# Kernel tuning notes

Measured on AMD Instinct MI355X. Metric: run time of the kernel, lower is better.

Reference implementation:

```python
import jax, jax.numpy as jnp
import numpy as np

N = 50000
E = 800000
IN = 256
HEADS = 8
C = 32  # out_size // heads
OUT = HEADS * C
NEG_SLOPE = 0.2
LN_EPS = 1e-5


def setup_inputs() -> dict:
    key = jax.random.key(0)
    ks = jax.random.split(key, 6)
    x = jax.random.normal(ks[0], (N, IN), dtype=jnp.float32)
    edge_index = jax.random.randint(ks[1], (2, E), 0, N, dtype=jnp.int64)
    W = jax.random.normal(ks[2], (IN, OUT), dtype=jnp.float32) / np.sqrt(IN)
    att_src = jax.random.normal(ks[3], (HEADS, C), dtype=jnp.float32) / np.sqrt(C)
    att_dst = jax.random.normal(ks[4], (HEADS, C), dtype=jnp.float32) / np.sqrt(C)
    bias = jnp.zeros((OUT,), dtype=jnp.float32)
    ln_gamma = jnp.ones((OUT,), dtype=jnp.float32)
    ln_beta = jnp.zeros((OUT,), dtype=jnp.float32)
    return {"x": x, "edge_index": edge_index, "W": W, "att_src": att_src,
            "att_dst": att_dst, "bias": bias, "ln_gamma": ln_gamma, "ln_beta": ln_beta}


def _gat_layer(x, src, dst, W, att_src, att_dst, bias, ln_gamma, ln_beta):
    n = x.shape[0]
    h = (x @ W).reshape(n, HEADS, C)                      # [N,H,C]
    a_src = jnp.sum(h * att_src[None], axis=-1)           # [N,H]
    a_dst = jnp.sum(h * att_dst[None], axis=-1)           # [N,H]
    e = a_src[src] + a_dst[dst]                           # [Etot,H]
    e = jnp.where(e > 0, e, NEG_SLOPE * e)                # LeakyReLU(0.2)
    # segment softmax over incoming edges of each dst node
    emax = jax.lax.stop_gradient(jax.ops.segment_max(e, dst, num_segments=n))
    ex = jnp.exp(e - emax[dst])
    denom = jax.ops.segment_sum(ex, dst, num_segments=n)
    alpha = ex / denom[dst]                               # [Etot,H]
    msg = h[src] * alpha[:, :, None]                      # [Etot,H,C]
    out = jax.ops.segment_sum(msg, dst, num_segments=n).reshape(n, OUT) + bias
    # LayerNorm
    mu = jnp.mean(out, axis=-1, keepdims=True)
    var = jnp.var(out, axis=-1, keepdims=True)
    out = (out - mu) * jax.lax.rsqrt(var + LN_EPS) * ln_gamma + ln_beta
    return jax.nn.relu(out)


def reference(x, edge_index, W, att_src, att_dst, bias, ln_gamma, ln_beta):
    n = x.shape[0]
    loops = jnp.arange(n, dtype=edge_index.dtype)
    src = jnp.concatenate([edge_index[0], loops])  # PyG GATConv adds self-loops
    dst = jnp.concatenate([edge_index[1], loops])
    return _gat_layer(x, src, dst, W, att_src, att_dst, bias, ln_gamma, ln_beta)
```

## Files before the change

### kernel.cpp

```cpp
#include <hip/hip_runtime.h>

#define NEG 0.2f
#define ELLW 64

typedef __attribute__((ext_vector_type(8))) __bf16 bf16x8;
typedef __attribute__((ext_vector_type(4))) float f32x4;

__device__ __forceinline__ unsigned short f2bf(float f) {
    unsigned int u = __float_as_uint(f);
    u += 0x7FFFu + ((u >> 16) & 1u);
    return (unsigned short)(u >> 16);
}

__global__ __launch_bounds__(256) void prep_kernel(const float* __restrict__ W,
                                                   unsigned short* __restrict__ Wt,
                                                   int* __restrict__ len, int N) {
    int n = blockIdx.x, k = threadIdx.x;
    Wt[n * 256 + k] = f2bf(W[k * 256 + n]);
    int idx = n * 256 + k;
    if (idx < N) len[idx] = 0;
}

struct SmemGemm { unsigned short A[64][40]; unsigned short B[256][40]; };
struct SmemEpi  { float asrc[64][9]; float adst[64][9]; };
union SmemU { SmemGemm g; SmemEpi e; };

__global__ __launch_bounds__(256) void gemm_ell(const float* __restrict__ x,
                                                const unsigned short* __restrict__ Wt,
                                                unsigned short* __restrict__ h,
                                                const float* __restrict__ att_src,
                                                const float* __restrict__ att_dst,
                                                float* __restrict__ a_src,
                                                float* __restrict__ a_dst, int nrows, int G,
                                                const int* __restrict__ ei,
                                                int* __restrict__ len,
                                                int* __restrict__ ell, int E) {
    __shared__ SmemU sm;

    if (blockIdx.x >= G) {
        int e = (blockIdx.x - G) * 256 + threadIdx.x;
        if (e < E) {
            int s = ei[e], d = ei[E + e];
            int slot = atomicAdd(&len[d], 1);
            if (slot < ELLW) ell[d * ELLW + slot] = s;
        }
        return;
    }

    int t = threadIdx.x;
    int lane = t & 63, wave = t >> 6;
    int row0 = blockIdx.x * 64;

    f32x4 acc[4][4] = {};

    for (int kk = 0; kk < 8; ++kk) {
        int k0 = kk * 32;
        {
            int r = t >> 2, cg = (t & 3) * 8;
            int gr = row0 + r;
            float4 v0 = make_float4(0.f, 0.f, 0.f, 0.f), v1 = v0;
            if (gr < nrows) {
                const float* p = x + (size_t)gr * 256 + k0 + cg;
                v0 = *(const float4*)p;
                v1 = *(const float4*)(p + 4);
            }
            unsigned long long p0 = (unsigned long long)f2bf(v0.x)
                                  | ((unsigned long long)f2bf(v0.y) << 16)
                                  | ((unsigned long long)f2bf(v0.z) << 32)
                                  | ((unsigned long long)f2bf(v0.w) << 48);
            unsigned long long p1 = (unsigned long long)f2bf(v1.x)
                                  | ((unsigned long long)f2bf(v1.y) << 16)
                                  | ((unsigned long long)f2bf(v1.z) << 32)
                                  | ((unsigned long long)f2bf(v1.w) << 48);
            *(unsigned long long*)&sm.g.A[r][cg]     = p0;
            *(unsigned long long*)&sm.g.A[r][cg + 4] = p1;
        }
        {
            const uint4* src = (const uint4*)(Wt + (size_t)t * 256 + k0);
            uint4 b0 = src[0], b1 = src[1], b2 = src[2], b3 = src[3];
            *(uint4*)&sm.g.B[t][0]  = b0;
            *(uint4*)&sm.g.B[t][8]  = b1;
            *(uint4*)&sm.g.B[t][16] = b2;
            *(uint4*)&sm.g.B[t][24] = b3;
        }
        __syncthreads();

        int fr = lane & 15, fk = (lane >> 4) * 8;
        bf16x8 a[4];
#pragma unroll
        for (int mi = 0; mi < 4; ++mi) a[mi] = *(const bf16x8*)&sm.g.A[mi * 16 + fr][fk];
#pragma unroll
        for (int ni = 0; ni < 4; ++ni) {
            bf16x8 b = *(const bf16x8*)&sm.g.B[wave * 64 + ni * 16 + fr][fk];
#pragma unroll
            for (int mi = 0; mi < 4; ++mi)
                acc[mi][ni] = __builtin_amdgcn_mfma_f32_16x16x32_bf16(a[mi], b, acc[mi][ni], 0, 0, 0);
        }
        __syncthreads();
    }

    int cr = (lane >> 4) * 4;
    int cc = lane & 15;
#pragma unroll
    for (int mi = 0; mi < 4; ++mi)
#pragma unroll
        for (int ni = 0; ni < 4; ++ni)
#pragma unroll
            for (int r = 0; r < 4; ++r) {
                int row = row0 + mi * 16 + cr + r;
                int col = wave * 64 + ni * 16 + cc;
                if (row < nrows) h[(size_t)row * 256 + col] = f2bf(acc[mi][ni][r]);
            }

    float avs[4], avd[4];
#pragma unroll
    for (int ni = 0; ni < 4; ++ni) {
        int col = wave * 64 + ni * 16 + cc;
        avs[ni] = att_src[col];
        avd[ni] = att_dst[col];
    }
#pragma unroll
    for (int mi = 0; mi < 4; ++mi)
#pragma unroll
        for (int r = 0; r < 4; ++r) {
            float s0 = acc[mi][0][r] * avs[0] + acc[mi][1][r] * avs[1];
            float s1 = acc[mi][2][r] * avs[2] + acc[mi][3][r] * avs[3];
            float d0 = acc[mi][0][r] * avd[0] + acc[mi][1][r] * avd[1];
            float d1 = acc[mi][2][r] * avd[2] + acc[mi][3][r] * avd[3];
#pragma unroll
            for (int o = 1; o < 16; o <<= 1) {
                s0 += __shfl_xor(s0, o, 64);
                s1 += __shfl_xor(s1, o, 64);
                d0 += __shfl_xor(d0, o, 64);
                d1 += __shfl_xor(d1, o, 64);
            }
            if (cc == 0) {
                int row = mi * 16 + cr + r;
                sm.e.asrc[row][wave * 2 + 0] = s0;
                sm.e.asrc[row][wave * 2 + 1] = s1;
                sm.e.adst[row][wave * 2 + 0] = d0;
                sm.e.adst[row][wave * 2 + 1] = d1;
            }
        }
    __syncthreads();
    for (int idx = t; idx < 512; idx += 256) {
        int row = idx >> 3, hd = idx & 7;
        if (row0 + row < nrows) {
            a_src[(size_t)(row0 + row) * 8 + hd] = sm.e.asrc[row][hd];
            a_dst[(size_t)(row0 + row) * 8 + hd] = sm.e.adst[row][hd];
        }
    }
}

__global__ __launch_bounds__(256) void agg_kernel(const unsigned short* __restrict__ h,
                                                  const float* __restrict__ a_src,
                                                  const float* __restrict__ a_dst,
                                                  const int* __restrict__ len,
                                                  const int* __restrict__ ell,
                                                  const float* __restrict__ bias,
                                                  const float* __restrict__ gamma,
                                                  const float* __restrict__ beta,
                                                  float* __restrict__ out) {
    int i = blockIdx.x;
    int t = threadIdx.x;
    int lane = t & 63, wave = t >> 6;
    int hh = t & 7, jj = t >> 3;
    int deg = len[i];
    deg = deg < ELLW ? deg : ELLW;

    __shared__ float al_buf[ELLW][8];
    __shared__ int   s_buf[ELLW];
    __shared__ float wred[4][8];
    __shared__ float ginv[8];
    __shared__ float al_self[8];
    __shared__ float partial[8][256];
    __shared__ float lnred[4][2];

    float adh = a_dst[i * 8 + hh];
    float es = a_src[i * 8 + hh] + adh;
    es = es > 0.f ? es : NEG * es;
    float esx = __expf(es);
    float sm = (jj == 0) ? esx : 0.f;
    if (t < 8) al_self[t] = esx;

#pragma unroll
    for (int it = 0; it < 2; ++it) {
        int j = it * 32 + jj;
        if (j < deg) {
            int s = ell[i * ELLW + j];
            if (hh == 0) s_buf[j] = s;
            float e = a_src[s * 8 + hh] + adh;
            e = e > 0.f ? e : NEG * e;
            float v = __expf(e);
            al_buf[j][hh] = v;
            sm += v;
        }
    }
    sm += __shfl_xor(sm, 8, 64);
    sm += __shfl_xor(sm, 16, 64);
    sm += __shfl_xor(sm, 32, 64);
    if (lane < 8) wred[wave][lane] = sm;
    __syncthreads();
    if (t < 8) ginv[t] = 1.0f / (wred[0][t] + wred[1][t] + wred[2][t] + wred[3][t]);
    __syncthreads();

    int sub = lane >> 5, l5 = lane & 31;
    int p = wave * 2 + sub;
    int c0 = l5 * 8;
    int hl = l5 >> 2;
    float invd = ginv[hl];
    f32x4 a0 = {0.f, 0.f, 0.f, 0.f}, a1 = {0.f, 0.f, 0.f, 0.f};
    for (int j = p; j < deg; j += 8) {
        int s = s_buf[j];
        float alpha = al_buf[j][hl] * invd;
        uint4 u = *(const uint4*)(h + (size_t)s * 256 + c0);
        a0[0] = fmaf(alpha, __uint_as_float(u.x << 16), a0[0]);
        a0[1] = fmaf(alpha, __uint_as_float(u.x & 0xffff0000u), a0[1]);
        a0[2] = fmaf(alpha, __uint_as_float(u.y << 16), a0[2]);
        a0[3] = fmaf(alpha, __uint_as_float(u.y & 0xffff0000u), a0[3]);
        a1[0] = fmaf(alpha, __uint_as_float(u.z << 16), a1[0]);
        a1[1] = fmaf(alpha, __uint_as_float(u.z & 0xffff0000u), a1[1]);
        a1[2] = fmaf(alpha, __uint_as_float(u.w << 16), a1[2]);
        a1[3] = fmaf(alpha, __uint_as_float(u.w & 0xffff0000u), a1[3]);
    }
    if (p == 7) {
        float alpha = al_self[hl] * invd;
        uint4 u = *(const uint4*)(h + (size_t)i * 256 + c0);
        a0[0] = fmaf(alpha, __uint_as_float(u.x << 16), a0[0]);
        a0[1] = fmaf(alpha, __uint_as_float(u.x & 0xffff0000u), a0[1]);
        a0[2] = fmaf(alpha, __uint_as_float(u.y << 16), a0[2]);
        a0[3] = fmaf(alpha, __uint_as_float(u.y & 0xffff0000u), a0[3]);
        a1[0] = fmaf(alpha, __uint_as_float(u.z << 16), a1[0]);
        a1[1] = fmaf(alpha, __uint_as_float(u.z & 0xffff0000u), a1[1]);
        a1[2] = fmaf(alpha, __uint_as_float(u.w << 16), a1[2]);
        a1[3] = fmaf(alpha, __uint_as_float(u.w & 0xffff0000u), a1[3]);
    }
    *(f32x4*)&partial[p][c0]     = a0;
    *(f32x4*)&partial[p][c0 + 4] = a1;
    __syncthreads();

    float o = bias[t];
#pragma unroll
    for (int q = 0; q < 8; ++q) o += partial[q][t];

    float s1 = o, s2 = o * o;
#pragma unroll
    for (int off = 32; off >= 1; off >>= 1) {
        s1 += __shfl_xor(s1, off, 64);
        s2 += __shfl_xor(s2, off, 64);
    }
    if (lane == 0) { lnred[wave][0] = s1; lnred[wave][1] = s2; }
    __syncthreads();
    float S1 = lnred[0][0] + lnred[1][0] + lnred[2][0] + lnred[3][0];
    float S2 = lnred[0][1] + lnred[1][1] + lnred[2][1] + lnred[3][1];
    float mean = S1 * (1.f / 256.f);
    float var = S2 * (1.f / 256.f) - mean * mean;
    float rstd = rsqrtf(var + 1e-5f);
    float val = (o - mean) * rstd * gamma[t] + beta[t];
    val = fmaxf(val, 0.f);
    out[(size_t)i * 256 + t] = val;
}

extern "C" void kernel_launch(void* const* d_in, const int* in_sizes, int n_in,
                              void* d_out, int out_size, void* d_ws, size_t ws_size,
                              hipStream_t stream) {
    const float* x       = (const float*)d_in[0];
    const int*   ei      = (const int*)d_in[1];
    const float* W       = (const float*)d_in[2];
    const float* att_src = (const float*)d_in[3];
    const float* att_dst = (const float*)d_in[4];
    const float* bias    = (const float*)d_in[5];
    const float* gamma   = (const float*)d_in[6];
    const float* beta    = (const float*)d_in[7];

    int N = in_sizes[0] / 256;
    int E = in_sizes[1] / 2;
    int G = (N + 63) / 64;
    int EB = (E + 255) / 256;

    char* ws = (char*)d_ws;
    size_t off = 0;
    auto alloc = [&](size_t bytes) -> void* {
        void* p = ws + off;
        off += (bytes + 255) & ~(size_t)255;
        return p;
    };
    unsigned short* Wt     = (unsigned short*)alloc((size_t)256 * 256 * 2);
    unsigned short* h      = (unsigned short*)alloc((size_t)N * 256 * 2);
    float*          a_src_ = (float*)alloc((size_t)N * 8 * 4);
    float*          a_dst_ = (float*)alloc((size_t)N * 8 * 4);
    int*            len    = (int*)alloc((size_t)N * 4);
    int*            ell    = (int*)alloc((size_t)N * ELLW * 4);

    prep_kernel<<<256, 256, 0, stream>>>(W, Wt, len, N);
    gemm_ell<<<G + EB, 256, 0, stream>>>(x, Wt, h, att_src, att_dst, a_src_, a_dst_, N, G,
                                         ei, len, ell, E);
    agg_kernel<<<N, 256, 0, stream>>>(h, a_src_, a_dst_, len, ell, bias, gamma, beta,
                                      (float*)d_out);
}
```

Baseline: 276.0 us.

## Load GEMM operands directly from global memory, drop prep kernel and LDS staging

Removes the W transpose/bf16 prep kernel and replaces it with a memset for the ELL length counters. The GEMM now loads x and W fragments straight from global memory into registers, converting fp32 to bf16 on the fly, with no shared-memory staging or barriers. This saves one kernel launch and the LDS round trip. In exchange each block re-reads W from global/L2 as strided scalar loads (8 per fragment), and operands are no longer shared across waves through LDS.

```diff
diff --git a/kernel.cpp b/kernel.cpp
--- a/kernel.cpp
+++ b/kernel.cpp
@@ -12,21 +12,12 @@
     return (unsigned short)(u >> 16);
 }
 
-__global__ __launch_bounds__(256) void prep_kernel(const float* __restrict__ W,
-                                                   unsigned short* __restrict__ Wt,
-                                                   int* __restrict__ len, int N) {
-    int n = blockIdx.x, k = threadIdx.x;
-    Wt[n * 256 + k] = f2bf(W[k * 256 + n]);
-    int idx = n * 256 + k;
-    if (idx < N) len[idx] = 0;
-}
-
-struct SmemGemm { unsigned short A[64][40]; unsigned short B[256][40]; };
-struct SmemEpi  { float asrc[64][9]; float adst[64][9]; };
-union SmemU { SmemGemm g; SmemEpi e; };
+union BF8 { bf16x8 v; unsigned short s[8]; };
+
+struct SmemEpi { float asrc[64][9]; float adst[64][9]; };
 
 __global__ __launch_bounds__(256) void gemm_ell(const float* __restrict__ x,
-                                                const unsigned short* __restrict__ Wt,
+                                                const float* __restrict__ W,
                                                 unsigned short* __restrict__ h,
                                                 const float* __restrict__ att_src,
                                                 const float* __restrict__ att_dst,
@@ -35,8 +26,6 @@
                                                 const int* __restrict__ ei,
                                                 int* __restrict__ len,
                                                 int* __restrict__ ell, int E) {
-    __shared__ SmemU sm;
-
     if (blockIdx.x >= G) {
         int e = (blockIdx.x - G) * 256 + threadIdx.x;
         if (e < E) {
@@ -47,56 +36,44 @@
         return;
     }
 
+    __shared__ SmemEpi sm;
+
     int t = threadIdx.x;
     int lane = t & 63, wave = t >> 6;
+    int quad = lane >> 4, fr = lane & 15;
     int row0 = blockIdx.x * 64;
 
     f32x4 acc[4][4] = {};
 
     for (int kk = 0; kk < 8; ++kk) {
         int k0 = kk * 32;
-        {
-            int r = t >> 2, cg = (t & 3) * 8;
-            int gr = row0 + r;
+        bf16x8 a[4];
+#pragma unroll
+        for (int mi = 0; mi < 4; ++mi) {
+            int row = row0 + mi * 16 + fr;
             float4 v0 = make_float4(0.f, 0.f, 0.f, 0.f), v1 = v0;
-            if (gr < nrows) {
-                const float* p = x + (size_t)gr * 256 + k0 + cg;
-                v0 = *(const float4*)p;
-                v1 = *(const float4*)(p + 4);
-            }
-            unsigned long long p0 = (unsigned long long)f2bf(v0.x)
-                                  | ((unsigned long long)f2bf(v0.y) << 16)
-                                  | ((unsigned long long)f2bf(v0.z) << 32)
-                                  | ((unsigned long long)f2bf(v0.w) << 48);
-            unsigned long long p1 = (unsigned long long)f2bf(v1.x)
-                                  | ((unsigned long long)f2bf(v1.y) << 16)
-                                  | ((unsigned long long)f2bf(v1.z) << 32)
-                                  | ((unsigned long long)f2bf(v1.w) << 48);
-            *(unsigned long long*)&sm.g.A[r][cg]     = p0;
-            *(unsigned long long*)&sm.g.A[r][cg + 4] = p1;
-        }
-        {
-            const uint4* src = (const uint4*)(Wt + (size_t)t * 256 + k0);
-            uint4 b0 = src[0], b1 = src[1], b2 = src[2], b3 = src[3];
-            *(uint4*)&sm.g.B[t][0]  = b0;
-            *(uint4*)&sm.g.B[t][8]  = b1;
-            *(uint4*)&sm.g.B[t][16] = b2;
-            *(uint4*)&sm.g.B[t][24] = b3;
-        }
-        __syncthreads();
-
-        int fr = lane & 15, fk = (lane >> 4) * 8;
-        bf16x8 a[4];
-#pragma unroll
-        for (int mi = 0; mi < 4; ++mi) a[mi] = *(const bf16x8*)&sm.g.A[mi * 16 + fr][fk];
+            if (row < nrows) {
+                const float* ap = x + (size_t)row * 256 + k0 + quad * 8;
+                v0 = *(const float4*)ap;
+                v1 = *(const float4*)(ap + 4);
+            }
+            BF8 u;
+            u.s[0] = f2bf(v0.x); u.s[1] = f2bf(v0.y); u.s[2] = f2bf(v0.z); u.s[3] = f2bf(v0.w);
+            u.s[4] = f2bf(v1.x); u.s[5] = f2bf(v1.y); u.s[6] = f2bf(v1.z); u.s[7] = f2bf(v1.w);
+            a[mi] = u.v;
+        }
 #pragma unroll
         for (int ni = 0; ni < 4; ++ni) {
-            bf16x8 b = *(const bf16x8*)&sm.g.B[wave * 64 + ni * 16 + fr][fk];
+            int n = wave * 64 + ni * 16 + fr;
+            const float* bp = W + (size_t)(k0 + quad * 8) * 256 + n;
+            BF8 u;
+#pragma unroll
+            for (int j = 0; j < 8; ++j) u.s[j] = f2bf(bp[j * 256]);
+            bf16x8 b = u.v;
 #pragma unroll
             for (int mi = 0; mi < 4; ++mi)
                 acc[mi][ni] = __builtin_amdgcn_mfma_f32_16x16x32_bf16(a[mi], b, acc[mi][ni], 0, 0, 0);
         }
-        __syncthreads();
     }
 
     int cr = (lane >> 4) * 4;
@@ -136,18 +113,18 @@
             }
             if (cc == 0) {
                 int row = mi * 16 + cr + r;
-                sm.e.asrc[row][wave * 2 + 0] = s0;
-                sm.e.asrc[row][wave * 2 + 1] = s1;
-                sm.e.adst[row][wave * 2 + 0] = d0;
-                sm.e.adst[row][wave * 2 + 1] = d1;
+                sm.asrc[row][wave * 2 + 0] = s0;
+                sm.asrc[row][wave * 2 + 1] = s1;
+                sm.adst[row][wave * 2 + 0] = d0;
+                sm.adst[row][wave * 2 + 1] = d1;
             }
         }
     __syncthreads();
     for (int idx = t; idx < 512; idx += 256) {
         int row = idx >> 3, hd = idx & 7;
         if (row0 + row < nrows) {
-            a_src[(size_t)(row0 + row) * 8 + hd] = sm.e.asrc[row][hd];
-            a_dst[(size_t)(row0 + row) * 8 + hd] = sm.e.adst[row][hd];
+            a_src[(size_t)(row0 + row) * 8 + hd] = sm.asrc[row][hd];
+            a_dst[(size_t)(row0 + row) * 8 + hd] = sm.adst[row][hd];
         }
     }
 }
@@ -285,15 +262,14 @@
         off += (bytes + 255) & ~(size_t)255;
         return p;
     };
-    unsigned short* Wt     = (unsigned short*)alloc((size_t)256 * 256 * 2);
     unsigned short* h      = (unsigned short*)alloc((size_t)N * 256 * 2);
     float*          a_src_ = (float*)alloc((size_t)N * 8 * 4);
     float*          a_dst_ = (float*)alloc((size_t)N * 8 * 4);
     int*            len    = (int*)alloc((size_t)N * 4);
     int*            ell    = (int*)alloc((size_t)N * ELLW * 4);
 
-    prep_kernel<<<256, 256, 0, stream>>>(W, Wt, len, N);
-    gemm_ell<<<G + EB, 256, 0, stream>>>(x, Wt, h, att_src, att_dst, a_src_, a_dst_, N, G,
+    hipMemsetAsync(len, 0, (size_t)N * 4, stream);
+    gemm_ell<<<G + EB, 256, 0, stream>>>(x, W, h, att_src, att_dst, a_src_, a_dst_, N, G,
                                          ei, len, ell, E);
     agg_kernel<<<N, 256, 0, stream>>>(h, a_src_, a_dst_, len, ell, bias, gamma, beta,
                                       (float*)d_out);
```

New measurement: 286.3 us. 1.04x slower.
